# Kernel optimization log

Measured on AMD Instinct MI355X. Metric: run time of the kernel, lower is better.

Reference implementation:

```python
import jax, jax.numpy as jnp
import numpy as np

NEG_SLOPE = 0.2
EPS = 1e-16

N_NODES = 50000
N_EDGES = 800000
IN_C = 256
HID_C = 64
HEADS = 4
OUT_C = 128
N_GRAPHS = 100


def setup_inputs() -> dict:
    key = jax.random.key(0)
    ks = jax.random.split(key, 12)
    x = jax.random.normal(ks[0], (N_NODES, IN_C), dtype=jnp.float32)
    edge_index = jax.random.randint(ks[1], (2, N_EDGES), 0, N_NODES, dtype=jnp.int64)
    batch = jnp.sort(jax.random.randint(ks[2], (N_NODES,), 0, N_GRAPHS, dtype=jnp.int64))
    s1 = 1.0 / np.sqrt(IN_C)
    s2 = 1.0 / np.sqrt(HEADS * HID_C)
    W1 = jax.random.uniform(ks[3], (IN_C, HEADS * HID_C), jnp.float32, -s1, s1)
    att_src1 = jax.random.uniform(ks[4], (HEADS, HID_C), jnp.float32, -s1, s1)
    att_dst1 = jax.random.uniform(ks[5], (HEADS, HID_C), jnp.float32, -s1, s1)
    bias1 = jnp.zeros((HEADS * HID_C,), jnp.float32)
    W2 = jax.random.uniform(ks[6], (HEADS * HID_C, OUT_C), jnp.float32, -s2, s2)
    att_src2 = jax.random.uniform(ks[7], (1, OUT_C), jnp.float32, -s2, s2)
    att_dst2 = jax.random.uniform(ks[8], (1, OUT_C), jnp.float32, -s2, s2)
    bias2 = jnp.zeros((OUT_C,), jnp.float32)
    return {"x": x, "W1": W1, "att_src1": att_src1, "att_dst1": att_dst1,
            "bias1": bias1, "W2": W2, "att_src2": att_src2, "att_dst2": att_dst2,
            "bias2": bias2, "edge_index": edge_index, "batch": batch,
            "num_graphs": N_GRAPHS}


def gat_conv(x, W, att_src, att_dst, bias, src, dst, heads, ch):
    # x: [N, F_in]; W: [F_in, heads*ch]; att_*: [heads, ch]
    n = x.shape[0]
    h = (x @ W).reshape(n, heads, ch)                      # [N, H, C]
    a_src = jnp.sum(h * att_src[None], axis=-1)            # [N, H]
    a_dst = jnp.sum(h * att_dst[None], axis=-1)            # [N, H]
    alpha = a_src[src] + a_dst[dst]                        # [E, H]
    alpha = jax.nn.leaky_relu(alpha, NEG_SLOPE)
    # segment softmax over destination nodes (every node has a self-loop)
    amax = jax.ops.segment_max(alpha, dst, num_segments=n)
    e = jnp.exp(alpha - amax[dst])
    denom = jax.ops.segment_sum(e, dst, num_segments=n)
    alpha = e / (denom[dst] + EPS)                         # [E, H]
    msg = h[src] * alpha[:, :, None]                       # [E, H, C]
    out = jax.ops.segment_sum(msg, dst, num_segments=n)    # [N, H, C]
    return out.reshape(n, heads * ch) + bias


def reference(x, W1, att_src1, att_dst1, bias1, W2, att_src2, att_dst2, bias2,
              edge_index, batch, num_graphs):
    n = x.shape[0]
    loops = jnp.arange(n, dtype=edge_index.dtype)
    src = jnp.concatenate([edge_index[0], loops])
    dst = jnp.concatenate([edge_index[1], loops])
    h = gat_conv(x, W1, att_src1, att_dst1, bias1, src, dst, HEADS, HID_C)
    h = jax.nn.relu(h)
    h = gat_conv(h, W2, att_src2, att_dst2, bias2, src, dst, 1, OUT_C)
    h = jax.nn.relu(h)
    # global mean pool over graphs
    sums = jax.ops.segment_sum(h, batch, num_segments=num_graphs)
    cnt = jax.ops.segment_sum(jnp.ones((n, 1), h.dtype), batch, num_segments=num_graphs)
    return sums / jnp.maximum(cnt, 1.0)
```

## Files before the change

### kernel.cpp

```cpp
#include <hip/hip_runtime.h>
#include <hip/hip_bf16.h>
#include <hip/hip_fp16.h>

#define N_NODES 50000
#define N_EDGES 800000
#define E_TOT   (N_EDGES + N_NODES)
#define IN_C    256
#define H1C     256
#define HEADS   4
#define HID_C   64
#define OUT_C   128
#define N_GRAPHS 100
#define NEG_SLOPE 0.2f
#define EPS_F 1e-16f
#define SCAN_BLOCKS 196

#define PREP_CAST_BLOCKS   12500
#define PREP_W1_BLOCKS     256
#define PREP_W2_BLOCKS     128
#define PREP_HIST_BLOCKS   3321
#define PREP_BOUNDS_BLOCKS 196
#define PREP_DOUT_BLOCKS   50
#define PREP_TOTAL (PREP_CAST_BLOCKS + PREP_W1_BLOCKS + PREP_W2_BLOCKS + PREP_HIST_BLOCKS + PREP_BOUNDS_BLOCKS + PREP_DOUT_BLOCKS)

typedef _Float16 half8_t __attribute__((ext_vector_type(8)));
typedef float f32x4 __attribute__((ext_vector_type(4)));

__global__ __launch_bounds__(256) void prep_kernel(const float* __restrict__ x,
                                                   _Float16* __restrict__ xh,
                                                   const float* __restrict__ W1,
                                                   _Float16* __restrict__ W1t,
                                                   const float* __restrict__ W2,
                                                   _Float16* __restrict__ W2t,
                                                   const int* __restrict__ ei,
                                                   int* __restrict__ hist,
                                                   const int* __restrict__ batch,
                                                   int* __restrict__ gstart,
                                                   float* __restrict__ d_out) {
    int b = blockIdx.x;
    int tid = threadIdx.x;
    if (b < PREP_CAST_BLOCKS) {
        int idx = b * 256 + tid;
        float4 v = reinterpret_cast<const float4*>(x)[idx];
        union { _Float16 h[4]; uint2 u; } p;
        p.h[0] = (_Float16)v.x; p.h[1] = (_Float16)v.y;
        p.h[2] = (_Float16)v.z; p.h[3] = (_Float16)v.w;
        reinterpret_cast<uint2*>(xh)[idx] = p.u;
        return;
    }
    b -= PREP_CAST_BLOCKS;
    if (b < PREP_W1_BLOCKS) {
        int idx = b * 256 + tid;
        int n = idx >> 8, k = idx & 255;
        W1t[idx] = (_Float16)W1[k * 256 + n];
        return;
    }
    b -= PREP_W1_BLOCKS;
    if (b < PREP_W2_BLOCKS) {
        int idx = b * 256 + tid;
        int n = idx >> 8, k = idx & 255;
        W2t[idx] = (_Float16)W2[k * 128 + n];
        return;
    }
    b -= PREP_W2_BLOCKS;
    if (b < PREP_HIST_BLOCKS) {
        int idx = b * 256 + tid;
        if (idx < N_EDGES) {
            int d = ei[N_EDGES + idx];
            if (d >= 0 && d < N_NODES) atomicAdd(&hist[d], 1);
        } else if (idx < E_TOT) {
            atomicAdd(&hist[idx - N_EDGES], 1);
        }
        return;
    }
    b -= PREP_HIST_BLOCKS;
    if (b < PREP_BOUNDS_BLOCKS) {
        int idx = b * 256 + tid;
        if (idx >= N_NODES) return;
        int g = batch[idx];
        if (g < 0) g = 0; if (g >= N_GRAPHS) g = N_GRAPHS - 1;
        if (idx == 0) {
            for (int j = 0; j <= g; ++j) gstart[j] = 0;
        } else {
            int gp = batch[idx - 1];
            if (gp < 0) gp = 0; if (gp >= N_GRAPHS) gp = N_GRAPHS - 1;
            for (int j = gp + 1; j <= g; ++j) gstart[j] = idx;
        }
        if (idx == N_NODES - 1) {
            for (int j = g + 1; j <= N_GRAPHS; ++j) gstart[j] = N_NODES;
        }
        return;
    }
    b -= PREP_BOUNDS_BLOCKS;
    {
        int idx = b * 256 + tid;
        if (idx < N_GRAPHS * 128) d_out[idx] = 0.f;
    }
}

__global__ __launch_bounds__(256) void scan_phase1(const int* __restrict__ hist,
                                                   int* __restrict__ blockSums) {
    __shared__ int lds[256];
    int idx = blockIdx.x * 256 + threadIdx.x;
    int v = (idx < N_NODES) ? hist[idx] : 0;
    lds[threadIdx.x] = v;
    __syncthreads();
#pragma unroll
    for (int off = 128; off > 0; off >>= 1) {
        if (threadIdx.x < off) lds[threadIdx.x] += lds[threadIdx.x + off];
        __syncthreads();
    }
    if (threadIdx.x == 0) blockSums[blockIdx.x] = lds[0];
}

__global__ __launch_bounds__(256) void scan_phase3(const int* __restrict__ hist,
                                                   const int* __restrict__ blockSums,
                                                   int* __restrict__ row_ptr,
                                                   int* __restrict__ row_fill) {
    __shared__ int lds[256];
    __shared__ int s_off;
    int b = blockIdx.x;
    int t = threadIdx.x;
    if (t < 64) {
        int acc = 0;
        for (int i = t; i < b; i += 64) acc += blockSums[i];
#pragma unroll
        for (int off = 32; off > 0; off >>= 1) acc += __shfl_down(acc, off);
        if (t == 0) s_off = acc;
    }
    int idx = b * 256 + t;
    int v = (idx < N_NODES) ? hist[idx] : 0;
    lds[t] = v;
    __syncthreads();
#pragma unroll
    for (int off = 1; off < 256; off <<= 1) {
        int u = (t >= off) ? lds[t - off] : 0;
        __syncthreads();
        lds[t] += u;
        __syncthreads();
    }
    int excl = lds[t] - v + s_off;
    if (idx < N_NODES) {
        row_ptr[idx] = excl;
        row_fill[idx] = excl;
    }
    if (idx == N_NODES - 1) row_ptr[N_NODES] = excl + v;
}

__global__ __launch_bounds__(256) void scatter_kernel(const int* __restrict__ ei,
                                                      int* __restrict__ row_fill,
                                                      int* __restrict__ ssrc) {
    int idx = blockIdx.x * 256 + threadIdx.x;
    if (idx < N_EDGES) {
        int s = ei[idx];
        int d = ei[N_EDGES + idx];
        if (s < 0 || s >= N_NODES || d < 0 || d >= N_NODES) return;
        int pos = atomicAdd(&row_fill[d], 1);
        if (pos >= 0 && pos < E_TOT) ssrc[pos] = s;
    } else if (idx < E_TOT) {
        int nd = idx - N_EDGES;
        int pos = atomicAdd(&row_fill[nd], 1);
        if (pos >= 0 && pos < E_TOT) ssrc[pos] = nd;
    }
}

__global__ __launch_bounds__(256) void gemm_mfma_kernel(const _Float16* __restrict__ A,
                                                        const _Float16* __restrict__ Bt,
                                                        _Float16* __restrict__ C,
                                                        int mode,
                                                        const float* __restrict__ attS,
                                                        const float* __restrict__ attD,
                                                        float* __restrict__ a_src_o,
                                                        float* __restrict__ a_dst_o,
                                                        int M, int N) {
    __shared__ _Float16 As[128][48];
    __shared__ _Float16 Bs[128][48];
    __shared__ float lds_ps[128];
    __shared__ float lds_pd[128];
    const int tid = threadIdx.x;
    const int tileM = blockIdx.x * 128;
    const int tileN = blockIdx.y * 128;
    const int w = tid >> 6, lane = tid & 63;
    const int wm = (w >> 1) * 64, wn = (w & 1) * 64;
    const int quad = lane >> 4, mlane = lane & 15;
    const int srow = tid >> 2;
    const int schunk = (tid & 3) * 8;

    f32x4 zero = {0.f, 0.f, 0.f, 0.f};
    f32x4 acc[4][4];
#pragma unroll
    for (int i = 0; i < 4; ++i)
#pragma unroll
        for (int j = 0; j < 4; ++j) acc[i][j] = zero;

    const uint4* Av = reinterpret_cast<const uint4*>(A);
    const uint4* Bv = reinterpret_cast<const uint4*>(Bt);
    const int r0 = tileM + srow, r1 = r0 + 64;
    const bool ok0 = r0 < M, ok1 = r1 < M;
    const int bn0 = tileN + srow, bn1 = bn0 + 64;
    const uint4 z4 = make_uint4(0, 0, 0, 0);

    for (int k0 = 0; k0 < 256; k0 += 32) {
        const int kc = (k0 >> 3) + (tid & 3);
        uint4 a0 = ok0 ? Av[(size_t)r0 * 32 + kc] : z4;
        uint4 a1 = ok1 ? Av[(size_t)r1 * 32 + kc] : z4;
        uint4 b0 = Bv[(size_t)bn0 * 32 + kc];
        uint4 b1 = Bv[(size_t)bn1 * 32 + kc];
        __syncthreads();
        *reinterpret_cast<uint4*>(&As[srow][schunk]) = a0;
        *reinterpret_cast<uint4*>(&As[srow + 64][schunk]) = a1;
        *reinterpret_cast<uint4*>(&Bs[srow][schunk]) = b0;
        *reinterpret_cast<uint4*>(&Bs[srow + 64][schunk]) = b1;
        __syncthreads();
        half8_t af[4], bf[4];
#pragma unroll
        for (int mt = 0; mt < 4; ++mt)
            af[mt] = *reinterpret_cast<const half8_t*>(&As[wm + mt * 16 + mlane][quad * 8]);
#pragma unroll
        for (int nt = 0; nt < 4; ++nt)
            bf[nt] = *reinterpret_cast<const half8_t*>(&Bs[wn + nt * 16 + mlane][quad * 8]);
#pragma unroll
        for (int mt = 0; mt < 4; ++mt)
#pragma unroll
            for (int nt = 0; nt < 4; ++nt)
                acc[mt][nt] = __builtin_amdgcn_mfma_f32_16x16x32_f16(af[mt], bf[nt], acc[mt][nt], 0, 0, 0);
    }
#pragma unroll
    for (int mt = 0; mt < 4; ++mt) {
#pragma unroll
        for (int i = 0; i < 4; ++i) {
            int row = tileM + wm + mt * 16 + quad * 4 + i;
            if (row < M) {
                _Float16* cp = C + (size_t)row * N + tileN + wn;
#pragma unroll
                for (int nt = 0; nt < 4; ++nt)
                    cp[nt * 16 + mlane] = (_Float16)acc[mt][nt][i];
            }
        }
    }
    if (mode == 1) {
        int hd = (tileN + wn) >> 6;
        float as[4], ad[4];
#pragma unroll
        for (int nt = 0; nt < 4; ++nt) {
            as[nt] = attS[hd * 64 + nt * 16 + mlane];
            ad[nt] = attD[hd * 64 + nt * 16 + mlane];
        }
#pragma unroll
        for (int mt = 0; mt < 4; ++mt) {
#pragma unroll
            for (int i = 0; i < 4; ++i) {
                float ps = acc[mt][0][i] * as[0] + acc[mt][1][i] * as[1]
                         + acc[mt][2][i] * as[2] + acc[mt][3][i] * as[3];
                float pd = acc[mt][0][i] * ad[0] + acc[mt][1][i] * ad[1]
                         + acc[mt][2][i] * ad[2] + acc[mt][3][i] * ad[3];
#pragma unroll
                for (int off = 1; off < 16; off <<= 1) {
                    ps += __shfl_xor(ps, off);
                    pd += __shfl_xor(pd, off);
                }
                if (mlane == 0) {
                    int row = tileM + wm + mt * 16 + quad * 4 + i;
                    if (row < M) {
                        a_src_o[row * 4 + hd] = ps;
                        a_dst_o[row * 4 + hd] = pd;
                    }
                }
            }
        }
    } else if (mode == 2) {
        float as[4], ad[4];
#pragma unroll
        for (int nt = 0; nt < 4; ++nt) {
            as[nt] = attS[wn + nt * 16 + mlane];
            ad[nt] = attD[wn + nt * 16 + mlane];
        }
        float psa[4][4], pda[4][4];
#pragma unroll
        for (int mt = 0; mt < 4; ++mt) {
#pragma unroll
            for (int i = 0; i < 4; ++i) {
                float ps = acc[mt][0][i] * as[0] + acc[mt][1][i] * as[1]
                         + acc[mt][2][i] * as[2] + acc[mt][3][i] * as[3];
                float pd = acc[mt][0][i] * ad[0] + acc[mt][1][i] * ad[1]
                         + acc[mt][2][i] * ad[2] + acc[mt][3][i] * ad[3];
#pragma unroll
                for (int off = 1; off < 16; off <<= 1) {
                    ps += __shfl_xor(ps, off);
                    pd += __shfl_xor(pd, off);
                }
                psa[mt][i] = ps; pda[mt][i] = pd;
            }
        }
        __syncthreads();
        if (wn == 0 && mlane == 0) {
#pragma unroll
            for (int mt = 0; mt < 4; ++mt)
#pragma unroll
                for (int i = 0; i < 4; ++i) {
                    int lr = wm + mt * 16 + quad * 4 + i;
                    lds_ps[lr] = psa[mt][i];
                    lds_pd[lr] = pda[mt][i];
                }
        }
        __syncthreads();
        if (wn == 64 && mlane == 0) {
#pragma unroll
            for (int mt = 0; mt < 4; ++mt)
#pragma unroll
                for (int i = 0; i < 4; ++i) {
                    int lr = wm + mt * 16 + quad * 4 + i;
                    int row = tileM + lr;
                    if (row < M) {
                        a_src_o[row] = psa[mt][i] + lds_ps[lr];
                        a_dst_o[row] = pda[mt][i] + lds_pd[lr];
                    }
                }
        }
    }
}

__device__ __forceinline__ float lrelu(float x) { return x > 0.f ? x : NEG_SLOPE * x; }

__global__ __launch_bounds__(256) void edge1_kernel(const int* __restrict__ row_ptr,
                                                    const int* __restrict__ ssrc,
                                                    const __half* __restrict__ h1h,
                                                    const float* __restrict__ a_src,
                                                    const float* __restrict__ a_dst,
                                                    const float* __restrict__ bias,
                                                    __half* __restrict__ out) {
    int node = blockIdx.x * 4 + (threadIdx.x >> 6);
    int lane = threadIdx.x & 63;
    int hf   = lane >> 5;
    int cl   = lane & 31;
    int hd   = cl >> 3;
    int start = row_ptr[node], end = row_ptr[node + 1];
    int em1 = end - 1;
    float adh = a_dst[node * 4 + hd];

    const uint4* h1v = reinterpret_cast<const uint4*>(h1h);
    float4 aA0 = make_float4(0.f,0.f,0.f,0.f), aA1 = make_float4(0.f,0.f,0.f,0.f);
    float4 aB0 = make_float4(0.f,0.f,0.f,0.f), aB1 = make_float4(0.f,0.f,0.f,0.f);
    float s = 0.f;
    for (int e = start; e < end; e += 4) {
        int e0 = e + hf;
        int e1 = e + 2 + hf;
        int i0 = ssrc[e0 <= em1 ? e0 : em1];
        int i1 = ssrc[e1 <= em1 ? e1 : em1];
        float r0 = a_src[i0 * 4 + hd];
        float r1 = a_src[i1 * 4 + hd];
        uint4 q0 = h1v[(size_t)i0 * 32 + cl];
        uint4 q1 = h1v[(size_t)i1 * 32 + cl];
        float w0 = (e0 < end) ? __expf(lrelu(r0 + adh)) : 0.f;
        float w1 = (e1 < end) ? __expf(lrelu(r1 + adh)) : 0.f;
        s += w0 + w1;
        float2 f;
        f = __half22float2(*reinterpret_cast<const __half2*>(&q0.x)); aA0.x += w0*f.x; aA0.y += w0*f.y;
        f = __half22float2(*reinterpret_cast<const __half2*>(&q0.y)); aA0.z += w0*f.x; aA0.w += w0*f.y;
        f = __half22float2(*reinterpret_cast<const __half2*>(&q0.z)); aA1.x += w0*f.x; aA1.y += w0*f.y;
        f = __half22float2(*reinterpret_cast<const __half2*>(&q0.w)); aA1.z += w0*f.x; aA1.w += w0*f.y;
        f = __half22float2(*reinterpret_cast<const __half2*>(&q1.x)); aB0.x += w1*f.x; aB0.y += w1*f.y;
        f = __half22float2(*reinterpret_cast<const __half2*>(&q1.y)); aB0.z += w1*f.x; aB0.w += w1*f.y;
        f = __half22float2(*reinterpret_cast<const __half2*>(&q1.z)); aB1.x += w1*f.x; aB1.y += w1*f.y;
        f = __half22float2(*reinterpret_cast<const __half2*>(&q1.w)); aB1.z += w1*f.x; aB1.w += w1*f.y;
    }
    float4 c0, c1;
    c0.x = aA0.x + aB0.x; c0.y = aA0.y + aB0.y; c0.z = aA0.z + aB0.z; c0.w = aA0.w + aB0.w;
    c1.x = aA1.x + aB1.x; c1.y = aA1.y + aB1.y; c1.z = aA1.z + aB1.z; c1.w = aA1.w + aB1.w;
    c0.x += __shfl_xor(c0.x, 32); c0.y += __shfl_xor(c0.y, 32);
    c0.z += __shfl_xor(c0.z, 32); c0.w += __shfl_xor(c0.w, 32);
    c1.x += __shfl_xor(c1.x, 32); c1.y += __shfl_xor(c1.y, 32);
    c1.z += __shfl_xor(c1.z, 32); c1.w += __shfl_xor(c1.w, 32);
    s += __shfl_xor(s, 32);
    float inv = 1.0f / (s + EPS_F);
    if (lane < 32) {
        const float4* b4 = reinterpret_cast<const float4*>(bias);
        float4 b0 = b4[cl * 2], b1 = b4[cl * 2 + 1];
        union { _Float16 h[8]; uint4 u; } st;
        st.h[0] = (_Float16)fmaxf(c0.x * inv + b0.x, 0.f);
        st.h[1] = (_Float16)fmaxf(c0.y * inv + b0.y, 0.f);
        st.h[2] = (_Float16)fmaxf(c0.z * inv + b0.z, 0.f);
        st.h[3] = (_Float16)fmaxf(c0.w * inv + b0.w, 0.f);
        st.h[4] = (_Float16)fmaxf(c1.x * inv + b1.x, 0.f);
        st.h[5] = (_Float16)fmaxf(c1.y * inv + b1.y, 0.f);
        st.h[6] = (_Float16)fmaxf(c1.z * inv + b1.z, 0.f);
        st.h[7] = (_Float16)fmaxf(c1.w * inv + b1.w, 0.f);
        reinterpret_cast<uint4*>(out)[(size_t)node * 32 + cl] = st.u;
    }
}

__global__ __launch_bounds__(256) void edge2_kernel(const int* __restrict__ row_ptr,
                                                    const int* __restrict__ ssrc,
                                                    const __half* __restrict__ h2h,
                                                    const float* __restrict__ a_src,
                                                    const float* __restrict__ a_dst,
                                                    const float* __restrict__ bias,
                                                    float* __restrict__ out) {
    int lane = threadIdx.x & 63;
    int node = blockIdx.x * 8 + ((threadIdx.x >> 6) << 1) + (lane >> 5);
    int sub  = (lane >> 4) & 1;
    int cl   = lane & 15;
    int start = row_ptr[node], end = row_ptr[node + 1];
    int em1 = end - 1;
    float ad = a_dst[node];

    const uint4* h2v = reinterpret_cast<const uint4*>(h2h);
    float4 aA0 = make_float4(0.f,0.f,0.f,0.f), aA1 = make_float4(0.f,0.f,0.f,0.f);
    float4 aB0 = make_float4(0.f,0.f,0.f,0.f), aB1 = make_float4(0.f,0.f,0.f,0.f);
    float s = 0.f;
    for (int e = start; e < end; e += 4) {
        int e0 = e + sub;
        int e1 = e + 2 + sub;
        int i0 = ssrc[e0 <= em1 ? e0 : em1];
        int i1 = ssrc[e1 <= em1 ? e1 : em1];
        float r0 = a_src[i0];
        float r1 = a_src[i1];
        uint4 q0 = h2v[(size_t)i0 * 16 + cl];
        uint4 q1 = h2v[(size_t)i1 * 16 + cl];
        float w0 = (e0 < end) ? __expf(lrelu(r0 + ad)) : 0.f;
        float w1 = (e1 < end) ? __expf(lrelu(r1 + ad)) : 0.f;
        s += w0 + w1;
        float2 f;
        f = __half22float2(*reinterpret_cast<const __half2*>(&q0.x)); aA0.x += w0*f.x; aA0.y += w0*f.y;
        f = __half22float2(*reinterpret_cast<const __half2*>(&q0.y)); aA0.z += w0*f.x; aA0.w += w0*f.y;
        f = __half22float2(*reinterpret_cast<const __half2*>(&q0.z)); aA1.x += w0*f.x; aA1.y += w0*f.y;
        f = __half22float2(*reinterpret_cast<const __half2*>(&q0.w)); aA1.z += w0*f.x; aA1.w += w0*f.y;
        f = __half22float2(*reinterpret_cast<const __half2*>(&q1.x)); aB0.x += w1*f.x; aB0.y += w1*f.y;
        f = __half22float2(*reinterpret_cast<const __half2*>(&q1.y)); aB0.z += w1*f.x; aB0.w += w1*f.y;
        f = __half22float2(*reinterpret_cast<const __half2*>(&q1.z)); aB1.x += w1*f.x; aB1.y += w1*f.y;
        f = __half22float2(*reinterpret_cast<const __half2*>(&q1.w)); aB1.z += w1*f.x; aB1.w += w1*f.y;
    }
    float4 c0, c1;
    c0.x = aA0.x + aB0.x; c0.y = aA0.y + aB0.y; c0.z = aA0.z + aB0.z; c0.w = aA0.w + aB0.w;
    c1.x = aA1.x + aB1.x; c1.y = aA1.y + aB1.y; c1.z = aA1.z + aB1.z; c1.w = aA1.w + aB1.w;
    c0.x += __shfl_xor(c0.x, 16); c0.y += __shfl_xor(c0.y, 16);
    c0.z += __shfl_xor(c0.z, 16); c0.w += __shfl_xor(c0.w, 16);
    c1.x += __shfl_xor(c1.x, 16); c1.y += __shfl_xor(c1.y, 16);
    c1.z += __shfl_xor(c1.z, 16); c1.w += __shfl_xor(c1.w, 16);
    s += __shfl_xor(s, 16);
    float inv = 1.0f / (s + EPS_F);
    if (sub == 0) {
        const float4* b4 = reinterpret_cast<const float4*>(bias);
        float4 b0 = b4[cl * 2], b1 = b4[cl * 2 + 1];
        float4 o0, o1;
        o0.x = fmaxf(c0.x * inv + b0.x, 0.f);
        o0.y = fmaxf(c0.y * inv + b0.y, 0.f);
        o0.z = fmaxf(c0.z * inv + b0.z, 0.f);
        o0.w = fmaxf(c0.w * inv + b0.w, 0.f);
        o1.x = fmaxf(c1.x * inv + b1.x, 0.f);
        o1.y = fmaxf(c1.y * inv + b1.y, 0.f);
        o1.z = fmaxf(c1.z * inv + b1.z, 0.f);
        o1.w = fmaxf(c1.w * inv + b1.w, 0.f);
        float4* o4 = reinterpret_cast<float4*>(out) + (size_t)node * 32 + cl * 2;
        o4[0] = o0;
        o4[1] = o1;
    }
}

#define POOL_CHUNK 64
__global__ __launch_bounds__(128) void pool_kernel(const float* __restrict__ out2,
                                                   const int* __restrict__ batch,
                                                   const int* __restrict__ gstart,
                                                   float* __restrict__ d_out) {
    int c = threadIdx.x;
    int node0 = blockIdx.x * POOL_CHUNK;
    int nodeEnd = node0 + POOL_CHUNK; if (nodeEnd > N_NODES) nodeEnd = N_NODES;
    if (node0 >= N_NODES) return;
    int gprev = batch[node0];
    float acc = 0.f;
    for (int node = node0; node < nodeEnd; ++node) {
        int g = batch[node];
        if (g != gprev) {
            if (gprev >= 0 && gprev < N_GRAPHS) {
                float cnt = (float)(gstart[gprev + 1] - gstart[gprev]);
                if (cnt < 1.f) cnt = 1.f;
                atomicAdd(&d_out[gprev * 128 + c], acc / cnt);
            }
            acc = 0.f;
            gprev = g;
        }
        acc += out2[(size_t)node * 128 + c];
    }
    if (gprev >= 0 && gprev < N_GRAPHS) {
        float cnt = (float)(gstart[gprev + 1] - gstart[gprev]);
        if (cnt < 1.f) cnt = 1.f;
        atomicAdd(&d_out[gprev * 128 + c], acc / cnt);
    }
}

extern "C" void kernel_launch(void* const* d_in, const int* in_sizes, int n_in,
                              void* d_out_v, int out_size, void* d_ws, size_t ws_size,
                              hipStream_t stream) {
    const float* x      = (const float*)d_in[0];
    const float* W1     = (const float*)d_in[1];
    const float* att_s1 = (const float*)d_in[2];
    const float* att_d1 = (const float*)d_in[3];
    const float* bias1  = (const float*)d_in[4];
    const float* W2     = (const float*)d_in[5];
    const float* att_s2 = (const float*)d_in[6];
    const float* att_d2 = (const float*)d_in[7];
    const float* bias2  = (const float*)d_in[8];
    const int*   ei     = (const int*)d_in[9];
    const int*   batch  = (const int*)d_in[10];
    float* d_out = (float*)d_out_v;

    float* ws = (float*)d_ws;
    _Float16* xh    = (_Float16*)ws;
    _Float16* h1h   = (_Float16*)(ws + 6400000);
    _Float16* out1h = (_Float16*)(ws + 12800000);
    _Float16* h2h   = (_Float16*)ws;
    float*    out2  = ws + 6400000;
    float* a_src1 = ws + 19200000;
    float* a_dst1 = a_src1 + 200000;
    float* a_src2 = a_dst1 + 200000;
    float* a_dst2 = a_src2 + 50000;
    int* hist     = (int*)(a_dst2 + 50000);
    int* row_ptr  = hist + 50000;
    int* row_fill = row_ptr + 50016;
    int* ssrc     = row_fill + 50016;
    int* gstart   = ssrc + E_TOT;
    int* blockSums    = gstart + 128;
    int* blockOffsets = blockSums + SCAN_BLOCKS;
    _Float16* W1t = (_Float16*)(blockOffsets + 256);
    _Float16* W2t = W1t + 65536;

    hipMemsetAsync(hist, 0, N_NODES * sizeof(int), stream);

    prep_kernel<<<PREP_TOTAL, 256, 0, stream>>>(x, xh, W1, W1t, W2, W2t,
                                                ei, hist, batch, gstart, d_out);

    scan_phase1<<<SCAN_BLOCKS, 256, 0, stream>>>(hist, blockSums);
    scan_phase3<<<SCAN_BLOCKS, 256, 0, stream>>>(hist, blockSums, row_ptr, row_fill);
    scatter_kernel<<<(E_TOT + 255) / 256, 256, 0, stream>>>(ei, row_fill, ssrc);

    {
        dim3 g((N_NODES + 127) / 128, H1C / 128);
        gemm_mfma_kernel<<<g, 256, 0, stream>>>(xh, W1t, h1h, 1,
                                                att_s1, att_d1, a_src1, a_dst1,
                                                N_NODES, H1C);
    }
    edge1_kernel<<<N_NODES / 4, 256, 0, stream>>>(row_ptr, ssrc, (const __half*)h1h,
                                                  a_src1, a_dst1, bias1, (__half*)out1h);

    {
        dim3 g((N_NODES + 127) / 128, OUT_C / 128);
        gemm_mfma_kernel<<<g, 256, 0, stream>>>(out1h, W2t, h2h, 2,
                                                att_s2, att_d2, a_src2, a_dst2,
                                                N_NODES, OUT_C);
    }
    edge2_kernel<<<N_NODES / 8, 256, 0, stream>>>(row_ptr, ssrc, (const __half*)h2h,
                                                  a_src2, a_dst2, bias2, out2);

    pool_kernel<<<(N_NODES + POOL_CHUNK - 1) / POOL_CHUNK, 128, 0, stream>>>(out2, batch, gstart, d_out);
}
```

Baseline: 356.3 us.

## Split GAT edge aggregation into weight precompute and feature-sliced gather passes

Result: slower. 446.3 us (+25.2%).

```diff
diff --git a/kernel.cpp b/kernel.cpp
--- a/kernel.cpp
+++ b/kernel.cpp
@@ -5,6 +5,7 @@
 #define N_NODES 50000
 #define N_EDGES 800000
 #define E_TOT   (N_EDGES + N_NODES)
+#define E_PAD   850048
 #define IN_C    256
 #define H1C     256
 #define HEADS   4
@@ -322,138 +323,94 @@
 
 __device__ __forceinline__ float lrelu(float x) { return x > 0.f ? x : NEG_SLOPE * x; }
 
-__global__ __launch_bounds__(256) void edge1_kernel(const int* __restrict__ row_ptr,
+template<int NH>
+__global__ __launch_bounds__(256) void edgew_kernel(const int* __restrict__ row_ptr,
                                                     const int* __restrict__ ssrc,
-                                                    const __half* __restrict__ h1h,
                                                     const float* __restrict__ a_src,
                                                     const float* __restrict__ a_dst,
-                                                    const float* __restrict__ bias,
-                                                    __half* __restrict__ out) {
+                                                    float* __restrict__ wpl,
+                                                    float* __restrict__ spl) {
     int node = blockIdx.x * 4 + (threadIdx.x >> 6);
     int lane = threadIdx.x & 63;
-    int hf   = lane >> 5;
-    int cl   = lane & 31;
-    int hd   = cl >> 3;
     int start = row_ptr[node], end = row_ptr[node + 1];
-    int em1 = end - 1;
-    float adh = a_dst[node * 4 + hd];
-
-    const uint4* h1v = reinterpret_cast<const uint4*>(h1h);
-    float4 aA0 = make_float4(0.f,0.f,0.f,0.f), aA1 = make_float4(0.f,0.f,0.f,0.f);
-    float4 aB0 = make_float4(0.f,0.f,0.f,0.f), aB1 = make_float4(0.f,0.f,0.f,0.f);
-    float s = 0.f;
-    for (int e = start; e < end; e += 4) {
-        int e0 = e + hf;
-        int e1 = e + 2 + hf;
-        int i0 = ssrc[e0 <= em1 ? e0 : em1];
-        int i1 = ssrc[e1 <= em1 ? e1 : em1];
-        float r0 = a_src[i0 * 4 + hd];
-        float r1 = a_src[i1 * 4 + hd];
-        uint4 q0 = h1v[(size_t)i0 * 32 + cl];
-        uint4 q1 = h1v[(size_t)i1 * 32 + cl];
-        float w0 = (e0 < end) ? __expf(lrelu(r0 + adh)) : 0.f;
-        float w1 = (e1 < end) ? __expf(lrelu(r1 + adh)) : 0.f;
-        s += w0 + w1;
-        float2 f;
-        f = __half22float2(*reinterpret_cast<const __half2*>(&q0.x)); aA0.x += w0*f.x; aA0.y += w0*f.y;
-        f = __half22float2(*reinterpret_cast<const __half2*>(&q0.y)); aA0.z += w0*f.x; aA0.w += w0*f.y;
-        f = __half22float2(*reinterpret_cast<const __half2*>(&q0.z)); aA1.x += w0*f.x; aA1.y += w0*f.y;
-        f = __half22float2(*reinterpret_cast<const __half2*>(&q0.w)); aA1.z += w0*f.x; aA1.w += w0*f.y;
-        f = __half22float2(*reinterpret_cast<const __half2*>(&q1.x)); aB0.x += w1*f.x; aB0.y += w1*f.y;
-        f = __half22float2(*reinterpret_cast<const __half2*>(&q1.y)); aB0.z += w1*f.x; aB0.w += w1*f.y;
-        f = __half22float2(*reinterpret_cast<const __half2*>(&q1.z)); aB1.x += w1*f.x; aB1.y += w1*f.y;
-        f = __half22float2(*reinterpret_cast<const __half2*>(&q1.w)); aB1.z += w1*f.x; aB1.w += w1*f.y;
-    }
-    float4 c0, c1;
-    c0.x = aA0.x + aB0.x; c0.y = aA0.y + aB0.y; c0.z = aA0.z + aB0.z; c0.w = aA0.w + aB0.w;
-    c1.x = aA1.x + aB1.x; c1.y = aA1.y + aB1.y; c1.z = aA1.z + aB1.z; c1.w = aA1.w + aB1.w;
-    c0.x += __shfl_xor(c0.x, 32); c0.y += __shfl_xor(c0.y, 32);
-    c0.z += __shfl_xor(c0.z, 32); c0.w += __shfl_xor(c0.w, 32);
-    c1.x += __shfl_xor(c1.x, 32); c1.y += __shfl_xor(c1.y, 32);
-    c1.z += __shfl_xor(c1.z, 32); c1.w += __shfl_xor(c1.w, 32);
-    s += __shfl_xor(s, 32);
-    float inv = 1.0f / (s + EPS_F);
-    if (lane < 32) {
-        const float4* b4 = reinterpret_cast<const float4*>(bias);
-        float4 b0 = b4[cl * 2], b1 = b4[cl * 2 + 1];
-        union { _Float16 h[8]; uint4 u; } st;
-        st.h[0] = (_Float16)fmaxf(c0.x * inv + b0.x, 0.f);
-        st.h[1] = (_Float16)fmaxf(c0.y * inv + b0.y, 0.f);
-        st.h[2] = (_Float16)fmaxf(c0.z * inv + b0.z, 0.f);
-        st.h[3] = (_Float16)fmaxf(c0.w * inv + b0.w, 0.f);
-        st.h[4] = (_Float16)fmaxf(c1.x * inv + b1.x, 0.f);
-        st.h[5] = (_Float16)fmaxf(c1.y * inv + b1.y, 0.f);
-        st.h[6] = (_Float16)fmaxf(c1.z * inv + b1.z, 0.f);
-        st.h[7] = (_Float16)fmaxf(c1.w * inv + b1.w, 0.f);
-        reinterpret_cast<uint4*>(out)[(size_t)node * 32 + cl] = st.u;
-    }
-}
-
-__global__ __launch_bounds__(256) void edge2_kernel(const int* __restrict__ row_ptr,
-                                                    const int* __restrict__ ssrc,
-                                                    const __half* __restrict__ h2h,
-                                                    const float* __restrict__ a_src,
-                                                    const float* __restrict__ a_dst,
-                                                    const float* __restrict__ bias,
-                                                    float* __restrict__ out) {
+    float ad[NH], s[NH];
+#pragma unroll
+    for (int h = 0; h < NH; ++h) { ad[h] = a_dst[node * NH + h]; s[h] = 0.f; }
+    for (int e0 = start; e0 < end; e0 += 64) {
+        int e = e0 + lane;
+        bool v = e < end;
+        int ec = v ? e : end - 1;
+        int si = ssrc[ec];
+#pragma unroll
+        for (int h = 0; h < NH; ++h) {
+            float w = __expf(lrelu(a_src[si * NH + h] + ad[h]));
+            if (v) { wpl[h * E_PAD + e] = w; s[h] += w; }
+        }
+    }
+#pragma unroll
+    for (int off = 32; off > 0; off >>= 1)
+#pragma unroll
+        for (int h = 0; h < NH; ++h) s[h] += __shfl_xor(s[h], off);
+    if (lane == 0)
+#pragma unroll
+        for (int h = 0; h < NH; ++h) spl[h * 50016 + node] = s[h];
+}
+
+template<int ROW_U4, bool HALF_OUT>
+__global__ __launch_bounds__(256) void edgeagg_kernel(const int* __restrict__ row_ptr,
+                                                      const int* __restrict__ ssrc,
+                                                      const uint4* __restrict__ hrows,
+                                                      const float* __restrict__ wpl,
+                                                      const float* __restrict__ spl,
+                                                      const float* __restrict__ bias_sl,
+                                                      uint4* __restrict__ out_u4,
+                                                      float4* __restrict__ out_f4,
+                                                      int slice_u4) {
+    int node = blockIdx.x * 4 + (threadIdx.x >> 6);
     int lane = threadIdx.x & 63;
-    int node = blockIdx.x * 8 + ((threadIdx.x >> 6) << 1) + (lane >> 5);
-    int sub  = (lane >> 4) & 1;
-    int cl   = lane & 15;
-    int start = row_ptr[node], end = row_ptr[node + 1];
-    int em1 = end - 1;
-    float ad = a_dst[node];
-
-    const uint4* h2v = reinterpret_cast<const uint4*>(h2h);
-    float4 aA0 = make_float4(0.f,0.f,0.f,0.f), aA1 = make_float4(0.f,0.f,0.f,0.f);
-    float4 aB0 = make_float4(0.f,0.f,0.f,0.f), aB1 = make_float4(0.f,0.f,0.f,0.f);
-    float s = 0.f;
-    for (int e = start; e < end; e += 4) {
-        int e0 = e + sub;
-        int e1 = e + 2 + sub;
-        int i0 = ssrc[e0 <= em1 ? e0 : em1];
-        int i1 = ssrc[e1 <= em1 ? e1 : em1];
-        float r0 = a_src[i0];
-        float r1 = a_src[i1];
-        uint4 q0 = h2v[(size_t)i0 * 16 + cl];
-        uint4 q1 = h2v[(size_t)i1 * 16 + cl];
-        float w0 = (e0 < end) ? __expf(lrelu(r0 + ad)) : 0.f;
-        float w1 = (e1 < end) ? __expf(lrelu(r1 + ad)) : 0.f;
-        s += w0 + w1;
-        float2 f;
-        f = __half22float2(*reinterpret_cast<const __half2*>(&q0.x)); aA0.x += w0*f.x; aA0.y += w0*f.y;
-        f = __half22float2(*reinterpret_cast<const __half2*>(&q0.y)); aA0.z += w0*f.x; aA0.w += w0*f.y;
-        f = __half22float2(*reinterpret_cast<const __half2*>(&q0.z)); aA1.x += w0*f.x; aA1.y += w0*f.y;
-        f = __half22float2(*reinterpret_cast<const __half2*>(&q0.w)); aA1.z += w0*f.x; aA1.w += w0*f.y;
-        f = __half22float2(*reinterpret_cast<const __half2*>(&q1.x)); aB0.x += w1*f.x; aB0.y += w1*f.y;
-        f = __half22float2(*reinterpret_cast<const __half2*>(&q1.y)); aB0.z += w1*f.x; aB0.w += w1*f.y;
-        f = __half22float2(*reinterpret_cast<const __half2*>(&q1.z)); aB1.x += w1*f.x; aB1.y += w1*f.y;
-        f = __half22float2(*reinterpret_cast<const __half2*>(&q1.w)); aB1.z += w1*f.x; aB1.w += w1*f.y;
-    }
-    float4 c0, c1;
-    c0.x = aA0.x + aB0.x; c0.y = aA0.y + aB0.y; c0.z = aA0.z + aB0.z; c0.w = aA0.w + aB0.w;
-    c1.x = aA1.x + aB1.x; c1.y = aA1.y + aB1.y; c1.z = aA1.z + aB1.z; c1.w = aA1.w + aB1.w;
-    c0.x += __shfl_xor(c0.x, 16); c0.y += __shfl_xor(c0.y, 16);
-    c0.z += __shfl_xor(c0.z, 16); c0.w += __shfl_xor(c0.w, 16);
-    c1.x += __shfl_xor(c1.x, 16); c1.y += __shfl_xor(c1.y, 16);
-    c1.z += __shfl_xor(c1.z, 16); c1.w += __shfl_xor(c1.w, 16);
-    s += __shfl_xor(s, 16);
-    float inv = 1.0f / (s + EPS_F);
-    if (sub == 0) {
-        const float4* b4 = reinterpret_cast<const float4*>(bias);
-        float4 b0 = b4[cl * 2], b1 = b4[cl * 2 + 1];
-        float4 o0, o1;
-        o0.x = fmaxf(c0.x * inv + b0.x, 0.f);
-        o0.y = fmaxf(c0.y * inv + b0.y, 0.f);
-        o0.z = fmaxf(c0.z * inv + b0.z, 0.f);
-        o0.w = fmaxf(c0.w * inv + b0.w, 0.f);
-        o1.x = fmaxf(c1.x * inv + b1.x, 0.f);
-        o1.y = fmaxf(c1.y * inv + b1.y, 0.f);
-        o1.z = fmaxf(c1.z * inv + b1.z, 0.f);
-        o1.w = fmaxf(c1.w * inv + b1.w, 0.f);
-        float4* o4 = reinterpret_cast<float4*>(out) + (size_t)node * 32 + cl * 2;
-        o4[0] = o0;
-        o4[1] = o1;
+    int eg = lane >> 3, cs = lane & 7;
+    int start = row_ptr[node], end = row_ptr[node + 1], em1 = end - 1;
+    float acc[8];
+#pragma unroll
+    for (int k = 0; k < 8; ++k) acc[k] = 0.f;
+    for (int e0 = start; e0 < end; e0 += 8) {
+        int e = e0 + eg;
+        int ec = e <= em1 ? e : em1;
+        int si = ssrc[ec];
+        float w = wpl[ec];
+        w = (e < end) ? w : 0.f;
+        uint4 q = hrows[(size_t)si * ROW_U4 + slice_u4 + cs];
+        const __half* qh = reinterpret_cast<const __half*>(&q);
+#pragma unroll
+        for (int k = 0; k < 8; ++k)
+            acc[k] = fmaf(__half2float(qh[k]), w, acc[k]);
+    }
+#pragma unroll
+    for (int off = 8; off < 64; off <<= 1)
+#pragma unroll
+        for (int k = 0; k < 8; ++k) acc[k] += __shfl_xor(acc[k], off);
+    float inv = 1.0f / (spl[node] + EPS_F);
+    if (lane < 8) {
+        if (HALF_OUT) {
+            union { _Float16 h[8]; uint4 u; } st;
+#pragma unroll
+            for (int k = 0; k < 8; ++k)
+                st.h[k] = (_Float16)fmaxf(acc[k] * inv + bias_sl[cs * 8 + k], 0.f);
+            out_u4[(size_t)node * ROW_U4 + slice_u4 + cs] = st.u;
+        } else {
+            float4 o0, o1;
+            o0.x = fmaxf(acc[0] * inv + bias_sl[cs * 8 + 0], 0.f);
+            o0.y = fmaxf(acc[1] * inv + bias_sl[cs * 8 + 1], 0.f);
+            o0.z = fmaxf(acc[2] * inv + bias_sl[cs * 8 + 2], 0.f);
+            o0.w = fmaxf(acc[3] * inv + bias_sl[cs * 8 + 3], 0.f);
+            o1.x = fmaxf(acc[4] * inv + bias_sl[cs * 8 + 4], 0.f);
+            o1.y = fmaxf(acc[5] * inv + bias_sl[cs * 8 + 5], 0.f);
+            o1.z = fmaxf(acc[6] * inv + bias_sl[cs * 8 + 6], 0.f);
+            o1.w = fmaxf(acc[7] * inv + bias_sl[cs * 8 + 7], 0.f);
+            float4* o4 = out_f4 + (size_t)node * 32 + slice_u4 * 2 + cs * 2;
+            o4[0] = o0;
+            o4[1] = o1;
+        }
     }
 }
 
@@ -510,6 +467,10 @@
     _Float16* out1h = (_Float16*)(ws + 12800000);
     _Float16* h2h   = (_Float16*)ws;
     float*    out2  = ws + 6400000;
+    float* w1pl   = ws;
+    float* s1pl   = ws + 4 * E_PAD;
+    float* w2pl   = ws + 3400192;
+    float* s2pl   = ws + 3400192 + E_PAD;
     float* a_src1 = ws + 19200000;
     float* a_dst1 = a_src1 + 200000;
     float* a_src2 = a_dst1 + 200000;
@@ -539,8 +500,13 @@
                                                 att_s1, att_d1, a_src1, a_dst1,
                                                 N_NODES, H1C);
     }
-    edge1_kernel<<<N_NODES / 4, 256, 0, stream>>>(row_ptr, ssrc, (const __half*)h1h,
-                                                  a_src1, a_dst1, bias1, (__half*)out1h);
+    edgew_kernel<4><<<N_NODES / 4, 256, 0, stream>>>(row_ptr, ssrc, a_src1, a_dst1,
+                                                     w1pl, s1pl);
+    for (int p = 0; p < 4; ++p) {
+        edgeagg_kernel<32, true><<<N_NODES / 4, 256, 0, stream>>>(
+            row_ptr, ssrc, (const uint4*)h1h, w1pl + p * E_PAD, s1pl + p * 50016,
+            bias1 + p * 64, (uint4*)out1h, nullptr, p * 8);
+    }
 
     {
         dim3 g((N_NODES + 127) / 128, OUT_C / 128);
@@ -548,8 +514,13 @@
                                                 att_s2, att_d2, a_src2, a_dst2,
                                                 N_NODES, OUT_C);
     }
-    edge2_kernel<<<N_NODES / 8, 256, 0, stream>>>(row_ptr, ssrc, (const __half*)h2h,
-                                                  a_src2, a_dst2, bias2, out2);
+    edgew_kernel<1><<<N_NODES / 4, 256, 0, stream>>>(row_ptr, ssrc, a_src2, a_dst2,
+                                                     w2pl, s2pl);
+    for (int p = 0; p < 2; ++p) {
+        edgeagg_kernel<16, false><<<N_NODES / 4, 256, 0, stream>>>(
+            row_ptr, ssrc, (const uint4*)h2h, w2pl, s2pl,
+            bias2 + p * 64, nullptr, (float4*)out2, p * 8);
+    }
 
     pool_kernel<<<(N_NODES + POOL_CHUNK - 1) / POOL_CHUNK, 128, 0, stream>>>(out2, batch, gstart, d_out);
 }
```

## Replace global-atomic CSR scatter with two-level LDS bucket sort

Applied to the files above, without the earlier changes.

Result: faster. 345.6 us (-3.0%).

```diff
diff --git a/kernel.cpp b/kernel.cpp
--- a/kernel.cpp
+++ b/kernel.cpp
@@ -14,6 +14,12 @@
 #define NEG_SLOPE 0.2f
 #define EPS_F 1e-16f
 #define SCAN_BLOCKS 196
+
+#define NBUCKET 391
+#define SORT_BLOCKS 104
+#define EDGES_PER_SB 8192
+#define BH_STRIDE 392
+#define STAGE_CAP 3072
 
 #define PREP_CAST_BLOCKS   12500
 #define PREP_W1_BLOCKS     256
@@ -115,8 +121,7 @@
 
 __global__ __launch_bounds__(256) void scan_phase3(const int* __restrict__ hist,
                                                    const int* __restrict__ blockSums,
-                                                   int* __restrict__ row_ptr,
-                                                   int* __restrict__ row_fill) {
+                                                   int* __restrict__ row_ptr) {
     __shared__ int lds[256];
     __shared__ int s_off;
     int b = blockIdx.x;
@@ -140,27 +145,99 @@
         __syncthreads();
     }
     int excl = lds[t] - v + s_off;
-    if (idx < N_NODES) {
-        row_ptr[idx] = excl;
-        row_fill[idx] = excl;
-    }
+    if (idx < N_NODES) row_ptr[idx] = excl;
     if (idx == N_NODES - 1) row_ptr[N_NODES] = excl + v;
 }
 
-__global__ __launch_bounds__(256) void scatter_kernel(const int* __restrict__ ei,
-                                                      int* __restrict__ row_fill,
-                                                      int* __restrict__ ssrc) {
-    int idx = blockIdx.x * 256 + threadIdx.x;
-    if (idx < N_EDGES) {
-        int s = ei[idx];
-        int d = ei[N_EDGES + idx];
-        if (s < 0 || s >= N_NODES || d < 0 || d >= N_NODES) return;
-        int pos = atomicAdd(&row_fill[d], 1);
-        if (pos >= 0 && pos < E_TOT) ssrc[pos] = s;
-    } else if (idx < E_TOT) {
-        int nd = idx - N_EDGES;
-        int pos = atomicAdd(&row_fill[nd], 1);
-        if (pos >= 0 && pos < E_TOT) ssrc[pos] = nd;
+__global__ __launch_bounds__(256) void bucket_hist(const int* __restrict__ ei,
+                                                   int* __restrict__ bhist) {
+    __shared__ int bh[NBUCKET];
+    int tid = threadIdx.x;
+    for (int t = tid; t < NBUCKET; t += 256) bh[t] = 0;
+    __syncthreads();
+    int base = blockIdx.x * EDGES_PER_SB;
+#pragma unroll 4
+    for (int k = 0; k < EDGES_PER_SB / 256; ++k) {
+        int idx = base + k * 256 + tid;
+        int d = -1;
+        if (idx < N_EDGES) d = ei[N_EDGES + idx];
+        else if (idx < E_TOT) d = idx - N_EDGES;
+        if (d >= 0 && d < N_NODES) atomicAdd(&bh[d >> 7], 1);
+    }
+    __syncthreads();
+    for (int t = tid; t < NBUCKET; t += 256)
+        bhist[blockIdx.x * BH_STRIDE + t] = bh[t];
+}
+
+__global__ __launch_bounds__(64) void bucket_scan(int* __restrict__ bhist) {
+    int j = blockIdx.x;
+    int lane = threadIdx.x;
+    int carry = 0;
+    for (int b0 = 0; b0 < SORT_BLOCKS; b0 += 64) {
+        int b = b0 + lane;
+        int v = (b < SORT_BLOCKS) ? bhist[b * BH_STRIDE + j] : 0;
+        int inc = v;
+#pragma unroll
+        for (int off = 1; off < 64; off <<= 1) {
+            int u = __shfl_up(inc, off);
+            if (lane >= off) inc += u;
+        }
+        if (b < SORT_BLOCKS) bhist[b * BH_STRIDE + j] = inc - v + carry;
+        carry += __shfl(inc, 63);
+    }
+}
+
+__global__ __launch_bounds__(256) void bucket_bin(const int* __restrict__ ei,
+                                                  const int* __restrict__ row_ptr,
+                                                  const int* __restrict__ bhist,
+                                                  int* __restrict__ ebuf) {
+    __shared__ int cur[NBUCKET];
+    int tid = threadIdx.x;
+    for (int t = tid; t < NBUCKET; t += 256)
+        cur[t] = row_ptr[t << 7] + bhist[blockIdx.x * BH_STRIDE + t];
+    __syncthreads();
+    int base = blockIdx.x * EDGES_PER_SB;
+#pragma unroll 4
+    for (int k = 0; k < EDGES_PER_SB / 256; ++k) {
+        int idx = base + k * 256 + tid;
+        int s = 0, d = -1;
+        if (idx < N_EDGES) { s = ei[idx]; d = ei[N_EDGES + idx]; }
+        else if (idx < E_TOT) { s = idx - N_EDGES; d = s; }
+        if (d >= 0 && d < N_NODES) {
+            int p = atomicAdd(&cur[d >> 7], 1);
+            ebuf[p] = (s & 0xFFFF) | ((d & 127) << 16);
+        }
+    }
+}
+
+__global__ __launch_bounds__(256) void bucket_sort(const int* __restrict__ row_ptr,
+                                                   const int* __restrict__ ebuf,
+                                                   int* __restrict__ ssrc) {
+    __shared__ int cur2[128];
+    __shared__ int stage[STAGE_CAP];
+    int j = blockIdx.x;
+    int tid = threadIdx.x;
+    int jn0 = j << 7;
+    int nEnd = jn0 + 128; if (nEnd > N_NODES) nEnd = N_NODES;
+    int lo = row_ptr[jn0];
+    int hi = row_ptr[nEnd];
+    int span = hi - lo;
+    if (tid < nEnd - jn0) cur2[tid] = row_ptr[jn0 + tid] - lo;
+    __syncthreads();
+    if (span <= STAGE_CAP) {
+        for (int t = lo + tid; t < hi; t += 256) {
+            int v = ebuf[t];
+            int p = atomicAdd(&cur2[v >> 16], 1);
+            stage[p] = v & 0xFFFF;
+        }
+        __syncthreads();
+        for (int t = tid; t < span; t += 256) ssrc[lo + t] = stage[t];
+    } else {
+        for (int t = lo + tid; t < hi; t += 256) {
+            int v = ebuf[t];
+            int p = atomicAdd(&cur2[v >> 16], 1);
+            ssrc[lo + p] = v & 0xFFFF;
+        }
     }
 }
 
@@ -516,12 +593,12 @@
     float* a_dst2 = a_src2 + 50000;
     int* hist     = (int*)(a_dst2 + 50000);
     int* row_ptr  = hist + 50000;
-    int* row_fill = row_ptr + 50016;
-    int* ssrc     = row_fill + 50016;
-    int* gstart   = ssrc + E_TOT;
-    int* blockSums    = gstart + 128;
-    int* blockOffsets = blockSums + SCAN_BLOCKS;
-    _Float16* W1t = (_Float16*)(blockOffsets + 256);
+    int* ssrc     = row_ptr + 50016;
+    int* ebuf     = ssrc + 850000;
+    int* bhist    = ebuf + 851968;
+    int* gstart   = bhist + (SORT_BLOCKS * BH_STRIDE);
+    int* blockSums = gstart + 128;
+    _Float16* W1t = (_Float16*)(blockSums + 256);
     _Float16* W2t = W1t + 65536;
 
     hipMemsetAsync(hist, 0, N_NODES * sizeof(int), stream);
@@ -530,8 +607,12 @@
                                                 ei, hist, batch, gstart, d_out);
 
     scan_phase1<<<SCAN_BLOCKS, 256, 0, stream>>>(hist, blockSums);
-    scan_phase3<<<SCAN_BLOCKS, 256, 0, stream>>>(hist, blockSums, row_ptr, row_fill);
-    scatter_kernel<<<(E_TOT + 255) / 256, 256, 0, stream>>>(ei, row_fill, ssrc);
+    scan_phase3<<<SCAN_BLOCKS, 256, 0, stream>>>(hist, blockSums, row_ptr);
+
+    bucket_hist<<<SORT_BLOCKS, 256, 0, stream>>>(ei, bhist);
+    bucket_scan<<<NBUCKET, 64, 0, stream>>>(bhist);
+    bucket_bin<<<SORT_BLOCKS, 256, 0, stream>>>(ei, row_ptr, bhist, ebuf);
+    bucket_sort<<<NBUCKET, 256, 0, stream>>>(row_ptr, ebuf, ssrc);
 
     {
         dim3 g((N_NODES + 127) / 128, H1C / 128);
```
